# Optimization experiments

Hardware: AMD Instinct MI355X
Metric: run time of the kernel (lower is better)

Reference implementation:

```python
import jax, jax.numpy as jnp
import numpy as np

B, C, M, T = 2, 512, 16, 128
H = 8
D = C // H  # 64, divisible by 4 for 2D RoPE
G = C // 4  # GroupNorm groups = 128
S = M * T


def group_norm(x, scale, bias, groups=G, eps=1e-5):
    b, c, m, t = x.shape
    xg = x.reshape(b, groups, c // groups, m, t)
    mu = xg.mean(axis=(2, 3, 4), keepdims=True)
    var = xg.var(axis=(2, 3, 4), keepdims=True)
    xn = ((xg - mu) * jax.lax.rsqrt(var + eps)).reshape(b, c, m, t)
    return xn * scale[None, :, None, None] + bias[None, :, None, None]


def dwsep_conv(x, dw, pw):
    # depthwise 3x3 (groups=C) then pointwise 1x1
    y = jax.lax.conv_general_dilated(
        x, dw, window_strides=(1, 1), padding='SAME',
        dimension_numbers=('NCHW', 'HWIO', 'NCHW'), feature_group_count=x.shape[1])
    return jnp.einsum('bcmt,cd->bdmt', y, pw)


def rope2d(x):
    # x: [B,H,M,T,D]; first D/2 dims rotated by freq index m, last D/2 by time index t
    d = x.shape[-1]
    dh = d // 2
    q = dh // 2
    inv = 1.0 / (10000.0 ** (jnp.arange(q, dtype=jnp.float32) / q))

    def rot(v, ang):
        h = v.shape[-1] // 2
        v1, v2 = v[..., :h], v[..., h:]
        c, s = jnp.cos(ang), jnp.sin(ang)
        return jnp.concatenate([v1 * c - v2 * s, v1 * s + v2 * c], axis=-1)

    ang_f = jnp.arange(x.shape[2], dtype=jnp.float32)[:, None] * inv  # [M,q]
    ang_t = jnp.arange(x.shape[3], dtype=jnp.float32)[:, None] * inv  # [T,q]
    xf = rot(x[..., :dh], ang_f[:, None, :])  # broadcast over T
    xt = rot(x[..., dh:], ang_t)
    return jnp.concatenate([xf, xt], axis=-1)


def setup_inputs() -> dict:
    key = jax.random.key(0)
    ks = jax.random.split(key, 14)
    s = 0.02
    return {
        'x': jax.random.normal(ks[0], (B, C, M, T), jnp.float32),
        'lengths': jax.random.randint(ks[1], (B,), T // 2, T + 1),
        'gn_scale': jnp.ones((C,), jnp.float32),
        'gn_bias': jnp.zeros((C,), jnp.float32),
        'dw_q': jax.random.normal(ks[2], (3, 3, 1, C), jnp.float32) * s,
        'dw_k': jax.random.normal(ks[3], (3, 3, 1, C), jnp.float32) * s,
        'dw_v': jax.random.normal(ks[4], (3, 3, 1, C), jnp.float32) * s,
        'pw_q': jax.random.normal(ks[5], (C, C), jnp.float32) * s,
        'pw_k': jax.random.normal(ks[6], (C, C), jnp.float32) * s,
        'pw_v': jax.random.normal(ks[7], (C, C), jnp.float32) * s,
        'attn_w': jax.random.normal(ks[8], (C, C), jnp.float32) * s,
        'attn_b': jnp.zeros((C,), jnp.float32),
        'out_w': jax.random.normal(ks[9], (C, C), jnp.float32) * s,
        'out_b': jnp.zeros((C,), jnp.float32),
    }


def reference(x, lengths, gn_scale, gn_bias, dw_q, dw_k, dw_v, pw_q, pw_k, pw_v,
              attn_w, attn_b, out_w, out_b):
    residual = x
    xn = group_norm(x, gn_scale, gn_bias)

    def to_heads(y):  # [B,C,M,T] -> [B,H,M,T,D]
        return y.reshape(B, H, D, M, T).transpose(0, 1, 3, 4, 2)

    q = rope2d(to_heads(dwsep_conv(xn, dw_q, pw_q)))
    k = rope2d(to_heads(dwsep_conv(xn, dw_k, pw_k)))
    v = to_heads(dwsep_conv(xn, dw_v, pw_v))

    q = q.reshape(B, H, S, D)
    k = k.reshape(B, H, S, D)
    v = v.reshape(B, H, S, D)

    scores = jnp.einsum('bhsd,bhkd->bhsk', q, k) / np.sqrt(D).astype(np.float32)
    valid_t = jnp.arange(T)[None, :] < lengths[:, None]        # [B,T]
    valid = jnp.tile(valid_t, (1, M))                          # [B,S], token idx = m*T + t
    scores = jnp.where(valid[:, None, None, :], scores, jnp.float32(-1e9))
    attn = jax.nn.softmax(scores, axis=-1)
    o = jnp.einsum('bhsk,bhkd->bhsd', attn, v)                 # [B,H,S,D]

    o = o.transpose(0, 2, 1, 3).reshape(B, S, C)
    o = o @ attn_w + attn_b                                    # block output proj
    o = o.reshape(B, M, T, C).transpose(0, 3, 1, 2)            # [B,C,M,T]
    out = jnp.einsum('bcmt,cd->bdmt', o, out_w) + out_b[None, :, None, None]
    return residual + out
```

## Files before the change

kernel.cpp:

```cpp
#include <hip/hip_runtime.h>
#include <math.h>

#define CCH 512
#define SSQ 2048
#define MTOT 4096

typedef __bf16 bf16;
typedef __bf16 bf16x8 __attribute__((ext_vector_type(8)));
typedef __bf16 bf16x4 __attribute__((ext_vector_type(4)));
typedef float  f32x4  __attribute__((ext_vector_type(4)));

#define AS1 __attribute__((address_space(1)))
#define AS3 __attribute__((address_space(3)))
__device__ __forceinline__ void glds16(const void* g, void* l) {
    __builtin_amdgcn_global_load_lds((const AS1 void*)g, (AS3 void*)l, 16, 0, 0);
}

__global__ __launch_bounds__(256) void gnw_kernel(const float* __restrict__ x,
        float* __restrict__ mu, float* __restrict__ rstd,
        const float* __restrict__ w0, const float* __restrict__ w1,
        const float* __restrict__ w2, const float* __restrict__ w3,
        const float* __restrict__ w4, bf16* __restrict__ wT) {
    __shared__ float smem[64*65];
    int tid = threadIdx.x;
    if (blockIdx.x < 256) {
        float* s_sum = smem;
        float* s_sq  = smem + 256;
        int bg = blockIdx.x;
        long base = (long)bg * 8192;
        float sum = 0.f, sq = 0.f;
#pragma unroll
        for (int r = 0; r < 32; ++r) {
            float v = x[base + r*256 + tid];
            sum += v; sq += v*v;
        }
        s_sum[tid] = sum; s_sq[tid] = sq;
        __syncthreads();
        for (int off = 128; off > 0; off >>= 1) {
            if (tid < off) { s_sum[tid] += s_sum[tid+off]; s_sq[tid] += s_sq[tid+off]; }
            __syncthreads();
        }
        if (tid == 0) {
            float m = s_sum[0] * (1.f/8192.f);
            float v = s_sq[0]  * (1.f/8192.f) - m*m;
            mu[bg] = m;
            rstd[bg] = rsqrtf(v + 1e-5f);
        }
    } else {
        int bid = blockIdx.x - 256;
        int z = bid >> 6, r2 = bid & 63;
        int k0 = (r2 >> 3)*64, n0 = (r2 & 7)*64;
        const float* srcs[5] = {w0, w1, w2, w3, w4};
        const float* W = srcs[z];
        bf16* D = wT + (long)z * (CCH*CCH);
        float (*t)[65] = (float(*)[65])smem;
        int cI = tid & 63, r4 = tid >> 6;
#pragma unroll
        for (int p = 0; p < 16; ++p) {
            int kr = p*4 + r4;
            t[kr][cI] = W[(long)(k0+kr)*CCH + n0 + cI];
        }
        __syncthreads();
#pragma unroll
        for (int p = 0; p < 16; ++p) {
            int nr = p*4 + r4;
            D[(long)(n0+nr)*CCH + k0 + cI] = (bf16)t[cI][nr];
        }
    }
}

__global__ void tn_kernel(const float* __restrict__ x, const float* __restrict__ mu,
                          const float* __restrict__ rstd, const float* __restrict__ gsc,
                          const float* __restrict__ gbs, bf16* __restrict__ xnT) {
    __shared__ float t[64][65];
    int s0 = blockIdx.x*64, c0 = blockIdx.y*64, b = blockIdx.z;
    int tid = threadIdx.x;
    int cI = tid & 63, r4 = tid >> 6;
#pragma unroll
    for (int p = 0; p < 16; ++p) {
        int cr = p*4 + r4;
        t[cr][cI] = x[((long)(b*CCH + c0 + cr))*SSQ + s0 + cI];
    }
    __syncthreads();
#pragma unroll
    for (int p = 0; p < 16; ++p) {
        int sr = p*4 + r4;
        int c = c0 + cI;
        int g = b*128 + (c >> 2);
        float v = (t[cI][sr] - mu[g]) * rstd[g] * gsc[c] + gbs[c];
        xnT[((long)(b*SSQ + s0 + sr))*CCH + c] = (bf16)v;
    }
}

__global__ __launch_bounds__(256) void dw3_kernel(const bf16* __restrict__ xnT,
        const float* __restrict__ dwq, const float* __restrict__ dwk,
        const float* __restrict__ dwv,
        bf16* __restrict__ yq, bf16* __restrict__ yk, bf16* __restrict__ yv) {
    int tid = threadIdx.x;
    int cc = (tid & 63) * 8;
    int s  = blockIdx.x*4 + (tid >> 6);
    int sl = s & (SSQ-1);
    int b  = s >> 11;
    int m = sl >> 7, t = sl & 127;
    float aq[8] = {}, ak[8] = {}, av[8] = {};
#pragma unroll
    for (int di = 0; di < 3; ++di) {
        int m2 = m + di - 1;
        if ((unsigned)m2 >= 16u) continue;
#pragma unroll
        for (int dj = 0; dj < 3; ++dj) {
            int t2 = t + dj - 1;
            if ((unsigned)t2 >= 128u) continue;
            bf16x8 xv = *(const bf16x8*)(xnT + ((long)(b*SSQ + m2*128 + t2))*CCH + cc);
            int wi = (di*3 + dj)*CCH + cc;
#pragma unroll
            for (int i = 0; i < 8; ++i) {
                float xf = (float)xv[i];
                aq[i] += xf * dwq[wi+i];
                ak[i] += xf * dwk[wi+i];
                av[i] += xf * dwv[wi+i];
            }
        }
    }
    bf16x8 oq, ok, ov;
#pragma unroll
    for (int i = 0; i < 8; ++i) { oq[i] = (bf16)aq[i]; ok[i] = (bf16)ak[i]; ov[i] = (bf16)av[i]; }
    long o = (long)s*CCH + cc;
    *(bf16x8*)(yq + o) = oq;
    *(bf16x8*)(yk + o) = ok;
    *(bf16x8*)(yv + o) = ov;
}

template<int NFR>
__device__ __forceinline__ void gemm_core128(const bf16* __restrict__ A,
        const bf16* __restrict__ Wt, int m0, int n0,
        bf16* As, bf16* Bs, f32x4 (&acc)[4][NFR]) {
    int tid = threadIdx.x, lane = tid & 63, wid = tid >> 6;
    int sw = wid & 1, nw = wid >> 1;
    int col = lane & 15, quad = lane >> 4;
    const char* gA[4]; char* ldsA[4];
#pragma unroll
    for (int p = 0; p < 4; ++p) {
        int ci = tid + p*256;
        int row = ci >> 3;
        int c = (ci & 7) ^ (row & 7);
        gA[p] = (const char*)A + ((long)(m0+row)*CCH + c*8)*2;
        ldsA[p] = (char*)As + ci*16;
    }
    const char* gB[NFR]; char* ldsB[NFR];
#pragma unroll
    for (int p = 0; p < NFR; ++p) {
        int ci = tid + p*256;
        int row = ci >> 3;
        int c = (ci & 7) ^ (row & 7);
        gB[p] = (const char*)Wt + ((long)(n0+row)*CCH + c*8)*2;
        ldsB[p] = (char*)Bs + ci*16;
    }
    int rowA = sw*64 + col;
    int rowB = nw*(NFR*16) + col;
    for (int k0 = 0; k0 < CCH; k0 += 64) {
        __syncthreads();
#pragma unroll
        for (int p = 0; p < 4; ++p)   glds16(gA[p] + k0*2, ldsA[p]);
#pragma unroll
        for (int p = 0; p < NFR; ++p) glds16(gB[p] + k0*2, ldsB[p]);
        __syncthreads();
        bf16x8 af[4][2], bfr[NFR][2];
#pragma unroll
        for (int mt = 0; mt < 4; ++mt) {
            int r = rowA + mt*16;
#pragma unroll
            for (int ks = 0; ks < 2; ++ks) {
                int c = (ks*4 + quad) ^ (r & 7);
                af[mt][ks] = *(const bf16x8*)((char*)As + r*128 + c*16);
            }
        }
#pragma unroll
        for (int nt = 0; nt < NFR; ++nt) {
            int r = rowB + nt*16;
#pragma unroll
            for (int ks = 0; ks < 2; ++ks) {
                int c = (ks*4 + quad) ^ (r & 7);
                bfr[nt][ks] = *(const bf16x8*)((char*)Bs + r*128 + c*16);
            }
        }
#pragma unroll
        for (int ks = 0; ks < 2; ++ks)
#pragma unroll
            for (int mt = 0; mt < 4; ++mt)
#pragma unroll
                for (int nt = 0; nt < NFR; ++nt)
                    acc[mt][nt] = __builtin_amdgcn_mfma_f32_16x16x32_bf16(
                        af[mt][ks], bfr[nt][ks], acc[mt][nt], 0,0,0);
    }
}

__global__ __launch_bounds__(256) void gemm_qkv(const bf16* __restrict__ Abase,
        const bf16* __restrict__ wT, bf16* __restrict__ qout,
        bf16* __restrict__ kout, bf16* __restrict__ vout) {
    __shared__ bf16 As[128*64];
    __shared__ bf16 Bs[128*64];
    int m0 = blockIdx.x*128, n0 = blockIdx.y*128, z = blockIdx.z;
    f32x4 acc[4][4] = {};
    gemm_core128<4>(Abase + (long)z*MTOT*CCH, wT + (long)z*CCH*CCH, m0, n0, As, Bs, acc);
    int tid = threadIdx.x, lane = tid & 63, wid = tid >> 6;
    int sw = wid & 1, nw = wid >> 1;
    int col = lane & 15, quad = lane >> 4;
    int nbase = n0 + nw*64;
    int mb = m0 + sw*64;
    if (z < 2) {
        bf16* outp = z ? kout : qout;
        const float sc = z ? 1.0f : 0.125f;
        float invf = __expf(-(float)col * 0.5756462732485114f);
#pragma unroll
        for (int mt = 0; mt < 4; ++mt)
#pragma unroll
            for (int r = 0; r < 4; ++r) {
                int row = mb + mt*16 + quad*4 + r;
                int sl = row & (SSQ-1);
#pragma unroll
                for (int half = 0; half < 2; ++half) {
                    float pos = half ? (float)(sl & 127) : (float)(sl >> 7);
                    float ang = pos * invf;
                    float sn, cs;
                    __sincosf(ang, &sn, &cs);
                    float x1 = acc[mt][half*2+0][r], x2 = acc[mt][half*2+1][r];
                    outp[(long)row*CCH + nbase + half*32 + col]      = (bf16)((x1*cs - x2*sn)*sc);
                    outp[(long)row*CCH + nbase + half*32 + 16 + col] = (bf16)((x1*sn + x2*cs)*sc);
                }
            }
    } else {
#pragma unroll
        for (int mt = 0; mt < 4; ++mt)
#pragma unroll
            for (int nt = 0; nt < 4; ++nt) {
                int n = nbase + nt*16 + col;
                int row0 = mb + mt*16 + quad*4;
                int b = row0 >> 11, sl0 = row0 & (SSQ-1);
                bf16x4 pk;
#pragma unroll
                for (int r = 0; r < 4; ++r) pk[r] = (bf16)acc[mt][nt][r];
                *(bf16x4*)(vout + ((long)(b*CCH + n))*SSQ + sl0) = pk;
            }
    }
}

template<int MODE>
__global__ __launch_bounds__(256) void gemm_bf16(const bf16* __restrict__ A,
        const bf16* __restrict__ Wt, const float* __restrict__ bias,
        const float* __restrict__ resid, void* __restrict__ outv) {
    __shared__ bf16 As[128*64];
    __shared__ bf16 Bs[64*64];
    int m0 = blockIdx.x*128, n0 = blockIdx.y*64;
    f32x4 acc[4][2] = {};
    gemm_core128<2>(A, Wt, m0, n0, As, Bs, acc);
    int tid = threadIdx.x, lane = tid & 63, wid = tid >> 6;
    int sw = wid & 1, nw = wid >> 1;
    int col = lane & 15, quad = lane >> 4;
    int nb = n0 + nw*32, mb = m0 + sw*64;
    if (MODE == 3) {
        bf16* outp = (bf16*)outv;
#pragma unroll
        for (int nt = 0; nt < 2; ++nt) {
            int n = nb + nt*16 + col;
            float bv = bias[n];
#pragma unroll
            for (int mt = 0; mt < 4; ++mt)
#pragma unroll
                for (int r = 0; r < 4; ++r)
                    outp[(long)(mb + mt*16 + quad*4 + r)*CCH + n] = (bf16)(acc[mt][nt][r] + bv);
        }
    } else {
        float* outp = (float*)outv;
#pragma unroll
        for (int mt = 0; mt < 4; ++mt)
#pragma unroll
            for (int nt = 0; nt < 2; ++nt) {
                int n = nb + nt*16 + col;
                float bv = bias[n];
                int row0 = mb + mt*16 + quad*4;
                int b = row0 >> 11, sl0 = row0 & (SSQ-1);
                long off = ((long)(b*CCH + n))*SSQ + sl0;
                float4 rr = *(const float4*)(resid + off);
                float4 o4;
                o4.x = acc[mt][nt][0] + bv + rr.x;
                o4.y = acc[mt][nt][1] + bv + rr.y;
                o4.z = acc[mt][nt][2] + bv + rr.z;
                o4.w = acc[mt][nt][3] + bv + rr.w;
                *(float4*)(outp + off) = o4;
            }
    }
}

#define KIMG 8192
__global__ __launch_bounds__(256) void attn_kernel(
        const bf16* __restrict__ qb, const bf16* __restrict__ kb,
        const bf16* __restrict__ vb, const int* __restrict__ lengths,
        bf16* __restrict__ o) {
    __shared__ char KVs[2][2*KIMG];
    __shared__ bf16 Ps[4][16*72];
    int b = blockIdx.z, h = blockIdx.y;
    int tid = threadIdx.x, wid = tid >> 6, lane = tid & 63;
    int col = lane & 15, quad = lane >> 4;
    int q0 = blockIdx.x*64 + wid*16;
    int lenb = lengths[b];

    const char* gp[4]; long gstep[4]; int ldsoff[4];
#pragma unroll
    for (int p = 0; p < 4; ++p) {
        int idx = tid + p*256;
        int isV = idx >> 9;
        int rem = idx & 511;
        int r = rem >> 3;
        int csrc = (rem & 7) ^ (r & 7);
        if (!isV) { gp[p] = (const char*)kb + ((long)(b*SSQ + r))*1024 + h*128 + csrc*16; gstep[p] = 65536; }
        else      { gp[p] = (const char*)vb + ((long)(b*CCH + h*64 + r))*4096 + csrc*16;  gstep[p] = 128; }
        ldsoff[p] = idx*16;
    }

    f32x4 vm[2][4];
#pragma unroll
    for (int p2 = 0; p2 < 2; ++p2)
#pragma unroll
        for (int sub = 0; sub < 4; ++sub)
#pragma unroll
            for (int r = 0; r < 4; ++r)
                vm[p2][sub][r] = (p2*64 + sub*16 + quad*4 + r < lenb) ? 1.f : 0.f;

    const bf16* qp = qb + (long)(b*SSQ)*CCH + h*64;
    bf16x8 qf[2];
#pragma unroll
    for (int dc = 0; dc < 2; ++dc)
        qf[dc] = *(const bf16x8*)(qp + (long)(q0 + col)*CCH + dc*32 + quad*8);

    f32x4 of[4] = {};
    float lsum = 0.f;
    bf16* pw = Ps[wid];
    int cswz = col & 7;

    bf16x8 sreg[4];
#pragma unroll
    for (int p = 0; p < 4; ++p) sreg[p] = *(const bf16x8*)(gp[p]);
#pragma unroll
    for (int p = 0; p < 4; ++p) *(bf16x8*)(KVs[0] + ldsoff[p]) = sreg[p];
#pragma unroll
    for (int p = 0; p < 4; ++p) sreg[p] = *(const bf16x8*)(gp[p] + gstep[p]);
    __syncthreads();

    for (int t = 0; t < 32; ++t) {
        const bf16* K = (const bf16*)(KVs[t & 1]);
        const bf16* V = (const bf16*)(KVs[t & 1] + KIMG);
        int par = t & 1;
        f32x4 acc[4] = {};
#pragma unroll
        for (int sub = 0; sub < 4; ++sub)
#pragma unroll
            for (int dc = 0; dc < 2; ++dc) {
                bf16x8 kf = *(const bf16x8*)((const char*)K + (sub*16 + col)*128 + (((dc*4+quad) ^ cswz))*16);
                acc[sub] = __builtin_amdgcn_mfma_f32_16x16x32_bf16(kf, qf[dc], acc[sub], 0,0,0);
            }
#pragma unroll
        for (int sub = 0; sub < 4; ++sub) {
            bf16x4 pk;
#pragma unroll
            for (int r = 0; r < 4; ++r) {
                float p = __expf(acc[sub][r]) * vm[par][sub][r];
                lsum += p;
                pk[r] = (bf16)p;
            }
            *(bf16x4*)(pw + col*72 + sub*16 + quad*4) = pk;
        }
#pragma unroll
        for (int ks = 0; ks < 2; ++ks) {
            bf16x8 pf = *(const bf16x8*)(pw + col*72 + ks*32 + quad*8);
#pragma unroll
            for (int dt = 0; dt < 4; ++dt) {
                bf16x8 vf = *(const bf16x8*)((const char*)V + (dt*16 + col)*128 + (((ks*4+quad) ^ cswz))*16);
                of[dt] = __builtin_amdgcn_mfma_f32_16x16x32_bf16(pf, vf, of[dt], 0,0,0);
            }
        }
        if (t < 31) {
            char* nbuf = KVs[(t + 1) & 1];
#pragma unroll
            for (int p = 0; p < 4; ++p) *(bf16x8*)(nbuf + ldsoff[p]) = sreg[p];
            if (t < 30)
#pragma unroll
                for (int p = 0; p < 4; ++p)
                    sreg[p] = *(const bf16x8*)(gp[p] + (long)(t + 2) * gstep[p]);
        }
        __syncthreads();
    }
    lsum += __shfl_xor(lsum, 16);
    lsum += __shfl_xor(lsum, 32);
    float invl = 1.f / lsum;
    float ir[4];
#pragma unroll
    for (int r = 0; r < 4; ++r) ir[r] = __shfl(invl, quad*4 + r);
    bf16* ob = o + (long)(b*SSQ + q0)*CCH + h*64;
#pragma unroll
    for (int dt = 0; dt < 4; ++dt)
#pragma unroll
        for (int r = 0; r < 4; ++r)
            ob[(long)(quad*4 + r)*CCH + dt*16 + col] = (bf16)(of[dt][r] * ir[r]);
}

extern "C" void kernel_launch(void* const* d_in, const int* in_sizes, int n_in,
                              void* d_out, int out_size, void* d_ws, size_t ws_size,
                              hipStream_t stream) {
    const float* x        = (const float*)d_in[0];
    const int*   lengths  = (const int*)  d_in[1];
    const float* gn_scale = (const float*)d_in[2];
    const float* gn_bias  = (const float*)d_in[3];
    const float* dw_q     = (const float*)d_in[4];
    const float* dw_k     = (const float*)d_in[5];
    const float* dw_v     = (const float*)d_in[6];
    const float* pw_q     = (const float*)d_in[7];
    const float* pw_k     = (const float*)d_in[8];
    const float* pw_v     = (const float*)d_in[9];
    const float* attn_w   = (const float*)d_in[10];
    const float* attn_b   = (const float*)d_in[11];
    const float* out_w    = (const float*)d_in[12];
    const float* out_b    = (const float*)d_in[13];
    float* out = (float*)d_out;

    char* w = (char*)d_ws;
    float* mu   = (float*)w;
    float* rstd = (float*)(w + 1024);
    bf16* wT    = (bf16*)(w + 4096);
    bf16* wTa = wT + 3*CCH*CCH;
    bf16* wTo = wT + 4*CCH*CCH;
    bf16* xnT  = (bf16*)(w + 0x00300000);
    bf16* yT   = (bf16*)(w + 0x00700000);
    bf16* qbf  = (bf16*)(w + 0x01300000);
    bf16* kbf  = (bf16*)(w + 0x01700000);
    bf16* vbf  = (bf16*)(w + 0x01B00000);
    bf16* obf  = (bf16*)(w + 0x01F00000);
    bf16* tmpb = (bf16*)(w + 0x02300000);

    gnw_kernel<<<576, 256, 0, stream>>>(x, mu, rstd, pw_q, pw_k, pw_v, attn_w, out_w, wT);
    tn_kernel<<<dim3(32,8,2), 256, 0, stream>>>(x, mu, rstd, gn_scale, gn_bias, xnT);
    dw3_kernel<<<MTOT/4, 256, 0, stream>>>(xnT, dw_q, dw_k, dw_v,
                                           yT, yT + (long)MTOT*CCH, yT + (long)2*MTOT*CCH);

    gemm_qkv<<<dim3(MTOT/128, CCH/128, 3), 256, 0, stream>>>(yT, wT, qbf, kbf, vbf);

    attn_kernel<<<dim3(SSQ/64, 8, 2), 256, 0, stream>>>(qbf, kbf, vbf, lengths, obf);

    dim3 gg(MTOT/128, CCH/64);
    gemm_bf16<3><<<gg, 256, 0, stream>>>(obf, wTa, attn_b, nullptr, tmpb);
    gemm_bf16<4><<<gg, 256, 0, stream>>>(tmpb, wTo, out_b, x, out);
}
```

Baseline: 172.5 us.

## Split attention keys across warps with register-direct K/V loads; shrink QKV GEMM tile

The attention kernel now has each wave handle 32 queries against half of the 64 keys in each key tile. K and V fragments are loaded straight from global memory into registers with double buffering, so the LDS staging and per-tile block barriers are gone. The two key-halves are merged through shared memory at the end. Blocks are remapped so batch and head vary fastest, and the QKV GEMM uses 128x64 tiles, doubling its grid. The aim is fewer barriers, more parallelism and better L2 reuse, at the cost of duplicated global loads and more register pressure.

```diff
diff --git a/kernel.cpp b/kernel.cpp
--- a/kernel.cpp
+++ b/kernel.cpp
@@ -199,48 +199,45 @@
         const bf16* __restrict__ wT, bf16* __restrict__ qout,
         bf16* __restrict__ kout, bf16* __restrict__ vout) {
     __shared__ bf16 As[128*64];
-    __shared__ bf16 Bs[128*64];
-    int m0 = blockIdx.x*128, n0 = blockIdx.y*128, z = blockIdx.z;
-    f32x4 acc[4][4] = {};
-    gemm_core128<4>(Abase + (long)z*MTOT*CCH, wT + (long)z*CCH*CCH, m0, n0, As, Bs, acc);
+    __shared__ bf16 Bs[64*64];
+    int m0 = blockIdx.x*128, n0 = blockIdx.y*64, z = blockIdx.z;
+    f32x4 acc[4][2] = {};
+    gemm_core128<2>(Abase + (long)z*MTOT*CCH, wT + (long)z*CCH*CCH, m0, n0, As, Bs, acc);
     int tid = threadIdx.x, lane = tid & 63, wid = tid >> 6;
     int sw = wid & 1, nw = wid >> 1;
     int col = lane & 15, quad = lane >> 4;
-    int nbase = n0 + nw*64;
-    int mb = m0 + sw*64;
+    int nb = n0 + nw*32, mb = m0 + sw*64;
     if (z < 2) {
         bf16* outp = z ? kout : qout;
         const float sc = z ? 1.0f : 0.125f;
         float invf = __expf(-(float)col * 0.5756462732485114f);
+        bool tHalf = (nb & 32) != 0;
 #pragma unroll
         for (int mt = 0; mt < 4; ++mt)
 #pragma unroll
             for (int r = 0; r < 4; ++r) {
                 int row = mb + mt*16 + quad*4 + r;
                 int sl = row & (SSQ-1);
-#pragma unroll
-                for (int half = 0; half < 2; ++half) {
-                    float pos = half ? (float)(sl & 127) : (float)(sl >> 7);
-                    float ang = pos * invf;
-                    float sn, cs;
-                    __sincosf(ang, &sn, &cs);
-                    float x1 = acc[mt][half*2+0][r], x2 = acc[mt][half*2+1][r];
-                    outp[(long)row*CCH + nbase + half*32 + col]      = (bf16)((x1*cs - x2*sn)*sc);
-                    outp[(long)row*CCH + nbase + half*32 + 16 + col] = (bf16)((x1*sn + x2*cs)*sc);
-                }
+                float pos = tHalf ? (float)(sl & 127) : (float)(sl >> 7);
+                float ang = pos * invf;
+                float sn, cs;
+                __sincosf(ang, &sn, &cs);
+                float x1 = acc[mt][0][r], x2 = acc[mt][1][r];
+                outp[(long)row*CCH + nb + col]      = (bf16)((x1*cs - x2*sn)*sc);
+                outp[(long)row*CCH + nb + 16 + col] = (bf16)((x1*sn + x2*cs)*sc);
             }
     } else {
 #pragma unroll
         for (int mt = 0; mt < 4; ++mt)
 #pragma unroll
-            for (int nt = 0; nt < 4; ++nt) {
-                int n = nbase + nt*16 + col;
+            for (int nt = 0; nt < 2; ++nt) {
+                int n = nb + nt*16 + col;
                 int row0 = mb + mt*16 + quad*4;
-                int b = row0 >> 11, sl0 = row0 & (SSQ-1);
+                int bq = row0 >> 11, sl0 = row0 & (SSQ-1);
                 bf16x4 pk;
 #pragma unroll
                 for (int r = 0; r < 4; ++r) pk[r] = (bf16)acc[mt][nt][r];
-                *(bf16x4*)(vout + ((long)(b*CCH + n))*SSQ + sl0) = pk;
+                *(bf16x4*)(vout + ((long)(bq*CCH + n))*SSQ + sl0) = pk;
             }
     }
 }
@@ -292,116 +289,154 @@
     }
 }
 
-#define KIMG 8192
-__global__ __launch_bounds__(256) void attn_kernel(
+#define PSTR 40
+
+template<int MASKED>
+__device__ __forceinline__ void attn_tile(
+        const bf16x8 (&KC)[2][2], const bf16x8 (&VC)[4],
+        bf16x8 (&KN)[2][2], bf16x8 (&VN)[4], int tn,
+        const char* const (&kp)[2][2], const char* const (&vp)[4],
+        const bf16x8 (&qf)[2][2], const f32x4 (&vm)[2],
+        bf16* pw, int col, int quad,
+        f32x4 (&of)[2][4], float& ls0, float& ls1) {
+    if (tn < 32) {
+        long tko = (long)tn * 65536;
+#pragma unroll
+        for (int sub = 0; sub < 2; ++sub)
+#pragma unroll
+            for (int dc = 0; dc < 2; ++dc)
+                KN[sub][dc] = *(const bf16x8*)(kp[sub][dc] + tko);
+        long tvo = (long)tn * 128;
+#pragma unroll
+        for (int dt = 0; dt < 4; ++dt)
+            VN[dt] = *(const bf16x8*)(vp[dt] + tvo);
+    }
+    f32x4 sc[2][2] = {};
+#pragma unroll
+    for (int dc = 0; dc < 2; ++dc)
+#pragma unroll
+        for (int sub = 0; sub < 2; ++sub)
+#pragma unroll
+            for (int qt = 0; qt < 2; ++qt)
+                sc[sub][qt] = __builtin_amdgcn_mfma_f32_16x16x32_bf16(
+                    KC[sub][dc], qf[qt][dc], sc[sub][qt], 0,0,0);
+#pragma unroll
+    for (int sub = 0; sub < 2; ++sub)
+#pragma unroll
+        for (int qt = 0; qt < 2; ++qt) {
+            bf16x4 pk;
+#pragma unroll
+            for (int r = 0; r < 4; ++r) {
+                float p = __expf(sc[sub][qt][r]);
+                if (MASKED) p *= vm[sub][r];
+                if (qt) ls1 += p; else ls0 += p;
+                pk[r] = (bf16)p;
+            }
+            *(bf16x4*)(pw + (qt*16 + col)*PSTR + sub*16 + quad*4) = pk;
+        }
+    bf16x8 pf0 = *(const bf16x8*)(pw + col*PSTR + quad*8);
+    bf16x8 pf1 = *(const bf16x8*)(pw + (16 + col)*PSTR + quad*8);
+#pragma unroll
+    for (int dt = 0; dt < 4; ++dt) {
+        of[0][dt] = __builtin_amdgcn_mfma_f32_16x16x32_bf16(pf0, VC[dt], of[0][dt], 0,0,0);
+        of[1][dt] = __builtin_amdgcn_mfma_f32_16x16x32_bf16(pf1, VC[dt], of[1][dt], 0,0,0);
+    }
+}
+
+__global__ __launch_bounds__(256, 2) void attn_kernel(
         const bf16* __restrict__ qb, const bf16* __restrict__ kb,
         const bf16* __restrict__ vb, const int* __restrict__ lengths,
         bf16* __restrict__ o) {
-    __shared__ char KVs[2][2*KIMG];
-    __shared__ bf16 Ps[4][16*72];
-    int b = blockIdx.z, h = blockIdx.y;
+    __shared__ bf16 Ps[4][32*PSTR];
+    __shared__ float Om[2][2][4][16][17];
+    __shared__ float Lm[2][2][16];
+    int bid = blockIdx.x;
+    int bh = bid & 15, qtb = bid >> 4;
+    int h = bh >> 1, b = bh & 1;
     int tid = threadIdx.x, wid = tid >> 6, lane = tid & 63;
     int col = lane & 15, quad = lane >> 4;
-    int q0 = blockIdx.x*64 + wid*16;
+    int qh = wid & 1, kh = wid >> 1;
+    int q0 = qtb*64;
     int lenb = lengths[b];
 
-    const char* gp[4]; long gstep[4]; int ldsoff[4];
-#pragma unroll
-    for (int p = 0; p < 4; ++p) {
-        int idx = tid + p*256;
-        int isV = idx >> 9;
-        int rem = idx & 511;
-        int r = rem >> 3;
-        int csrc = (rem & 7) ^ (r & 7);
-        if (!isV) { gp[p] = (const char*)kb + ((long)(b*SSQ + r))*1024 + h*128 + csrc*16; gstep[p] = 65536; }
-        else      { gp[p] = (const char*)vb + ((long)(b*CCH + h*64 + r))*4096 + csrc*16;  gstep[p] = 128; }
-        ldsoff[p] = idx*16;
-    }
-
-    f32x4 vm[2][4];
-#pragma unroll
-    for (int p2 = 0; p2 < 2; ++p2)
-#pragma unroll
-        for (int sub = 0; sub < 4; ++sub)
-#pragma unroll
-            for (int r = 0; r < 4; ++r)
-                vm[p2][sub][r] = (p2*64 + sub*16 + quad*4 + r < lenb) ? 1.f : 0.f;
+    f32x4 vm[2];
+#pragma unroll
+    for (int sub = 0; sub < 2; ++sub)
+#pragma unroll
+        for (int r = 0; r < 4; ++r)
+            vm[sub][r] = (64 + kh*32 + sub*16 + quad*4 + r < lenb) ? 1.f : 0.f;
 
     const bf16* qp = qb + (long)(b*SSQ)*CCH + h*64;
-    bf16x8 qf[2];
-#pragma unroll
-    for (int dc = 0; dc < 2; ++dc)
-        qf[dc] = *(const bf16x8*)(qp + (long)(q0 + col)*CCH + dc*32 + quad*8);
-
-    f32x4 of[4] = {};
-    float lsum = 0.f;
+    bf16x8 qf[2][2];
+#pragma unroll
+    for (int qt = 0; qt < 2; ++qt)
+#pragma unroll
+        for (int dc = 0; dc < 2; ++dc)
+            qf[qt][dc] = *(const bf16x8*)(qp + (long)(q0 + qh*32 + qt*16 + col)*CCH + dc*32 + quad*8);
+
+    const char* kp[2][2];
+#pragma unroll
+    for (int sub = 0; sub < 2; ++sub)
+#pragma unroll
+        for (int dc = 0; dc < 2; ++dc)
+            kp[sub][dc] = (const char*)(kb + ((long)(b*SSQ + kh*32 + sub*16 + col))*CCH + h*64 + dc*32 + quad*8);
+    const char* vp[4];
+#pragma unroll
+    for (int dt = 0; dt < 4; ++dt)
+        vp[dt] = (const char*)(vb + ((long)(b*CCH + h*64 + dt*16 + col))*SSQ + kh*32 + quad*8);
+
+    f32x4 of[2][4] = {};
+    float ls0 = 0.f, ls1 = 0.f;
     bf16* pw = Ps[wid];
-    int cswz = col & 7;
-
-    bf16x8 sreg[4];
-#pragma unroll
-    for (int p = 0; p < 4; ++p) sreg[p] = *(const bf16x8*)(gp[p]);
-#pragma unroll
-    for (int p = 0; p < 4; ++p) *(bf16x8*)(KVs[0] + ldsoff[p]) = sreg[p];
-#pragma unroll
-    for (int p = 0; p < 4; ++p) sreg[p] = *(const bf16x8*)(gp[p] + gstep[p]);
+
+    bf16x8 kA[2][2], vA[4], kB[2][2], vB[4];
+#pragma unroll
+    for (int sub = 0; sub < 2; ++sub)
+#pragma unroll
+        for (int dc = 0; dc < 2; ++dc)
+            kA[sub][dc] = *(const bf16x8*)(kp[sub][dc]);
+#pragma unroll
+    for (int dt = 0; dt < 4; ++dt)
+        vA[dt] = *(const bf16x8*)(vp[dt]);
+
+    for (int t = 0; t < 32; t += 2) {
+        attn_tile<0>(kA, vA, kB, vB, t+1, kp, vp, qf, vm, pw, col, quad, of, ls0, ls1);
+        attn_tile<1>(kB, vB, kA, vA, t+2, kp, vp, qf, vm, pw, col, quad, of, ls0, ls1);
+    }
+
+    ls0 += __shfl_xor(ls0, 16); ls0 += __shfl_xor(ls0, 32);
+    ls1 += __shfl_xor(ls1, 16); ls1 += __shfl_xor(ls1, 32);
+
+    if (kh == 1) {
+#pragma unroll
+        for (int qt = 0; qt < 2; ++qt)
+#pragma unroll
+            for (int dt = 0; dt < 4; ++dt)
+#pragma unroll
+                for (int r = 0; r < 4; ++r)
+                    Om[qh][qt][dt][quad*4 + r][col] = of[qt][dt][r];
+        if (lane < 16) { Lm[qh][0][lane] = ls0; Lm[qh][1][lane] = ls1; }
+    }
     __syncthreads();
-
-    for (int t = 0; t < 32; ++t) {
-        const bf16* K = (const bf16*)(KVs[t & 1]);
-        const bf16* V = (const bf16*)(KVs[t & 1] + KIMG);
-        int par = t & 1;
-        f32x4 acc[4] = {};
-#pragma unroll
-        for (int sub = 0; sub < 4; ++sub)
-#pragma unroll
-            for (int dc = 0; dc < 2; ++dc) {
-                bf16x8 kf = *(const bf16x8*)((const char*)K + (sub*16 + col)*128 + (((dc*4+quad) ^ cswz))*16);
-                acc[sub] = __builtin_amdgcn_mfma_f32_16x16x32_bf16(kf, qf[dc], acc[sub], 0,0,0);
-            }
-#pragma unroll
-        for (int sub = 0; sub < 4; ++sub) {
-            bf16x4 pk;
-#pragma unroll
-            for (int r = 0; r < 4; ++r) {
-                float p = __expf(acc[sub][r]) * vm[par][sub][r];
-                lsum += p;
-                pk[r] = (bf16)p;
-            }
-            *(bf16x4*)(pw + col*72 + sub*16 + quad*4) = pk;
-        }
-#pragma unroll
-        for (int ks = 0; ks < 2; ++ks) {
-            bf16x8 pf = *(const bf16x8*)(pw + col*72 + ks*32 + quad*8);
-#pragma unroll
-            for (int dt = 0; dt < 4; ++dt) {
-                bf16x8 vf = *(const bf16x8*)((const char*)V + (dt*16 + col)*128 + (((ks*4+quad) ^ cswz))*16);
-                of[dt] = __builtin_amdgcn_mfma_f32_16x16x32_bf16(pf, vf, of[dt], 0,0,0);
-            }
-        }
-        if (t < 31) {
-            char* nbuf = KVs[(t + 1) & 1];
-#pragma unroll
-            for (int p = 0; p < 4; ++p) *(bf16x8*)(nbuf + ldsoff[p]) = sreg[p];
-            if (t < 30)
-#pragma unroll
-                for (int p = 0; p < 4; ++p)
-                    sreg[p] = *(const bf16x8*)(gp[p] + (long)(t + 2) * gstep[p]);
-        }
-        __syncthreads();
-    }
-    lsum += __shfl_xor(lsum, 16);
-    lsum += __shfl_xor(lsum, 32);
-    float invl = 1.f / lsum;
-    float ir[4];
-#pragma unroll
-    for (int r = 0; r < 4; ++r) ir[r] = __shfl(invl, quad*4 + r);
-    bf16* ob = o + (long)(b*SSQ + q0)*CCH + h*64;
-#pragma unroll
-    for (int dt = 0; dt < 4; ++dt)
-#pragma unroll
-        for (int r = 0; r < 4; ++r)
-            ob[(long)(quad*4 + r)*CCH + dt*16 + col] = (bf16)(of[dt][r] * ir[r]);
+    if (kh == 0) {
+        float i0 = 1.f / (ls0 + Lm[qh][0][col]);
+        float i1 = 1.f / (ls1 + Lm[qh][1][col]);
+        bf16* ob = o + (long)(b*SSQ + q0 + qh*32)*CCH + h*64;
+#pragma unroll
+        for (int qt = 0; qt < 2; ++qt) {
+            float inv = qt ? i1 : i0;
+            float ir[4];
+#pragma unroll
+            for (int r = 0; r < 4; ++r) ir[r] = __shfl(inv, quad*4 + r);
+#pragma unroll
+            for (int dt = 0; dt < 4; ++dt)
+#pragma unroll
+                for (int r = 0; r < 4; ++r) {
+                    float v = of[qt][dt][r] + Om[qh][qt][dt][quad*4 + r][col];
+                    ob[(long)(qt*16 + quad*4 + r)*CCH + dt*16 + col] = (bf16)(v * ir[r]);
+                }
+        }
+    }
 }
 
 extern "C" void kernel_launch(void* const* d_in, const int* in_sizes, int n_in,
@@ -442,9 +477,9 @@
     dw3_kernel<<<MTOT/4, 256, 0, stream>>>(xnT, dw_q, dw_k, dw_v,
                                            yT, yT + (long)MTOT*CCH, yT + (long)2*MTOT*CCH);
 
-    gemm_qkv<<<dim3(MTOT/128, CCH/128, 3), 256, 0, stream>>>(yT, wT, qbf, kbf, vbf);
-
-    attn_kernel<<<dim3(SSQ/64, 8, 2), 256, 0, stream>>>(qbf, kbf, vbf, lengths, obf);
+    gemm_qkv<<<dim3(MTOT/128, CCH/64, 3), 256, 0, stream>>>(yT, wT, qbf, kbf, vbf);
+
+    attn_kernel<<<512, 256, 0, stream>>>(qbf, kbf, vbf, lengths, obf);
 
     dim3 gg(MTOT/128, CCH/64);
     gemm_bf16<3><<<gg, 256, 0, stream>>>(obf, wTa, attn_b, nullptr, tmpb);
```

Measured after the change: 192.1 us. 11.3% more time.

## Split attention over KV halves, widen per-wave query tile, add merge kernel

Applied to the files above, without the earlier changes.

The attention kernel now splits the key range into two halves, giving 512 blocks over a flat grid. Each wave handles 32 queries, so every K/V fragment loaded from shared memory is reused twice. K/V tiles are loaded with asynchronous global-to-LDS loads, and the length mask becomes an additive bias applied only on masked tiles. A new merge kernel sums the fp32 partial outputs and row sums before normalising. The QKV GEMM is retiled to 128x64 for more blocks. The cost is extra fp32 partial traffic and one more launch.

```diff
diff --git a/kernel.cpp b/kernel.cpp
--- a/kernel.cpp
+++ b/kernel.cpp
@@ -199,48 +199,45 @@
         const bf16* __restrict__ wT, bf16* __restrict__ qout,
         bf16* __restrict__ kout, bf16* __restrict__ vout) {
     __shared__ bf16 As[128*64];
-    __shared__ bf16 Bs[128*64];
-    int m0 = blockIdx.x*128, n0 = blockIdx.y*128, z = blockIdx.z;
-    f32x4 acc[4][4] = {};
-    gemm_core128<4>(Abase + (long)z*MTOT*CCH, wT + (long)z*CCH*CCH, m0, n0, As, Bs, acc);
+    __shared__ bf16 Bs[64*64];
+    int m0 = blockIdx.x*128, n0 = blockIdx.y*64, z = blockIdx.z;
+    f32x4 acc[4][2] = {};
+    gemm_core128<2>(Abase + (long)z*MTOT*CCH, wT + (long)z*CCH*CCH, m0, n0, As, Bs, acc);
     int tid = threadIdx.x, lane = tid & 63, wid = tid >> 6;
     int sw = wid & 1, nw = wid >> 1;
     int col = lane & 15, quad = lane >> 4;
-    int nbase = n0 + nw*64;
-    int mb = m0 + sw*64;
+    int nb = n0 + nw*32, mb = m0 + sw*64;
     if (z < 2) {
         bf16* outp = z ? kout : qout;
         const float sc = z ? 1.0f : 0.125f;
         float invf = __expf(-(float)col * 0.5756462732485114f);
+        bool tHalf = (nb & 32) != 0;
 #pragma unroll
         for (int mt = 0; mt < 4; ++mt)
 #pragma unroll
             for (int r = 0; r < 4; ++r) {
                 int row = mb + mt*16 + quad*4 + r;
                 int sl = row & (SSQ-1);
-#pragma unroll
-                for (int half = 0; half < 2; ++half) {
-                    float pos = half ? (float)(sl & 127) : (float)(sl >> 7);
-                    float ang = pos * invf;
-                    float sn, cs;
-                    __sincosf(ang, &sn, &cs);
-                    float x1 = acc[mt][half*2+0][r], x2 = acc[mt][half*2+1][r];
-                    outp[(long)row*CCH + nbase + half*32 + col]      = (bf16)((x1*cs - x2*sn)*sc);
-                    outp[(long)row*CCH + nbase + half*32 + 16 + col] = (bf16)((x1*sn + x2*cs)*sc);
-                }
+                float pos = tHalf ? (float)(sl & 127) : (float)(sl >> 7);
+                float ang = pos * invf;
+                float sn, cs;
+                __sincosf(ang, &sn, &cs);
+                float x1 = acc[mt][0][r], x2 = acc[mt][1][r];
+                outp[(long)row*CCH + nb + col]      = (bf16)((x1*cs - x2*sn)*sc);
+                outp[(long)row*CCH + nb + 16 + col] = (bf16)((x1*sn + x2*cs)*sc);
             }
     } else {
 #pragma unroll
         for (int mt = 0; mt < 4; ++mt)
 #pragma unroll
-            for (int nt = 0; nt < 4; ++nt) {
-                int n = nbase + nt*16 + col;
+            for (int nt = 0; nt < 2; ++nt) {
+                int n = nb + nt*16 + col;
                 int row0 = mb + mt*16 + quad*4;
-                int b = row0 >> 11, sl0 = row0 & (SSQ-1);
+                int bq = row0 >> 11, sl0 = row0 & (SSQ-1);
                 bf16x4 pk;
 #pragma unroll
                 for (int r = 0; r < 4; ++r) pk[r] = (bf16)acc[mt][nt][r];
-                *(bf16x4*)(vout + ((long)(b*CCH + n))*SSQ + sl0) = pk;
+                *(bf16x4*)(vout + ((long)(bq*CCH + n))*SSQ + sl0) = pk;
             }
     }
 }
@@ -292,18 +289,22 @@
     }
 }
 
-#define KIMG 8192
 __global__ __launch_bounds__(256) void attn_kernel(
         const bf16* __restrict__ qb, const bf16* __restrict__ kb,
         const bf16* __restrict__ vb, const int* __restrict__ lengths,
-        bf16* __restrict__ o) {
-    __shared__ char KVs[2][2*KIMG];
-    __shared__ bf16 Ps[4][16*72];
-    int b = blockIdx.z, h = blockIdx.y;
+        float* __restrict__ opart, float* __restrict__ lpart) {
+    __shared__ char KV[2][16384];
+    __shared__ bf16 Ps[4][32*72];
+    int bid = blockIdx.x;
+    int bh = bid & 15;
+    int n  = bid >> 4;
+    int qt = n & 15, kvh = n >> 4;
+    int b = bh >> 3, h = bh & 7;
     int tid = threadIdx.x, wid = tid >> 6, lane = tid & 63;
     int col = lane & 15, quad = lane >> 4;
-    int q0 = blockIdx.x*64 + wid*16;
     int lenb = lengths[b];
+    int q0 = qt*128 + wid*32;
+    int k0 = kvh*1024;
 
     const char* gp[4]; long gstep[4]; int ldsoff[4];
 #pragma unroll
@@ -313,95 +314,122 @@
         int rem = idx & 511;
         int r = rem >> 3;
         int csrc = (rem & 7) ^ (r & 7);
-        if (!isV) { gp[p] = (const char*)kb + ((long)(b*SSQ + r))*1024 + h*128 + csrc*16; gstep[p] = 65536; }
-        else      { gp[p] = (const char*)vb + ((long)(b*CCH + h*64 + r))*4096 + csrc*16;  gstep[p] = 128; }
+        if (!isV) { gp[p] = (const char*)kb + ((long)(b*SSQ + k0 + r))*1024 + h*128 + csrc*16; gstep[p] = 65536; }
+        else      { gp[p] = (const char*)vb + ((long)(b*CCH + h*64 + r))*4096 + (long)k0*2 + csrc*16; gstep[p] = 128; }
         ldsoff[p] = idx*16;
     }
 
-    f32x4 vm[2][4];
-#pragma unroll
-    for (int p2 = 0; p2 < 2; ++p2)
-#pragma unroll
-        for (int sub = 0; sub < 4; ++sub)
-#pragma unroll
-            for (int r = 0; r < 4; ++r)
-                vm[p2][sub][r] = (p2*64 + sub*16 + quad*4 + r < lenb) ? 1.f : 0.f;
+    f32x4 mb[4];
+#pragma unroll
+    for (int sub = 0; sub < 4; ++sub)
+#pragma unroll
+        for (int r = 0; r < 4; ++r)
+            mb[sub][r] = (64 + sub*16 + quad*4 + r < lenb) ? 0.f : -10000.f;
 
     const bf16* qp = qb + (long)(b*SSQ)*CCH + h*64;
-    bf16x8 qf[2];
-#pragma unroll
-    for (int dc = 0; dc < 2; ++dc)
-        qf[dc] = *(const bf16x8*)(qp + (long)(q0 + col)*CCH + dc*32 + quad*8);
-
-    f32x4 of[4] = {};
-    float lsum = 0.f;
+    bf16x8 qf[2][2];
+#pragma unroll
+    for (int qt2 = 0; qt2 < 2; ++qt2)
+#pragma unroll
+        for (int dc = 0; dc < 2; ++dc)
+            qf[qt2][dc] = *(const bf16x8*)(qp + (long)(q0 + qt2*16 + col)*CCH + dc*32 + quad*8);
+
+    f32x4 of[2][4] = {};
+    float ls0 = 0.f, ls1 = 0.f;
     bf16* pw = Ps[wid];
     int cswz = col & 7;
 
-    bf16x8 sreg[4];
-#pragma unroll
-    for (int p = 0; p < 4; ++p) sreg[p] = *(const bf16x8*)(gp[p]);
-#pragma unroll
-    for (int p = 0; p < 4; ++p) *(bf16x8*)(KVs[0] + ldsoff[p]) = sreg[p];
-#pragma unroll
-    for (int p = 0; p < 4; ++p) sreg[p] = *(const bf16x8*)(gp[p] + gstep[p]);
+#pragma unroll
+    for (int p = 0; p < 4; ++p) glds16(gp[p], KV[0] + ldsoff[p]);
     __syncthreads();
 
-    for (int t = 0; t < 32; ++t) {
-        const bf16* K = (const bf16*)(KVs[t & 1]);
-        const bf16* V = (const bf16*)(KVs[t & 1] + KIMG);
-        int par = t & 1;
-        f32x4 acc[4] = {};
+    for (int t = 0; t < 16; ++t) {
+        if (t < 15) {
+#pragma unroll
+            for (int p = 0; p < 4; ++p)
+                glds16(gp[p] + (long)(t+1)*gstep[p], KV[(t+1) & 1] + ldsoff[p]);
+        }
+        const bf16* K = (const bf16*)(KV[t & 1]);
+        const bf16* V = (const bf16*)(KV[t & 1] + 8192);
+        bool masked = ((kvh*16 + t) & 1) != 0;
+        f32x4 sc[4][2];
+#pragma unroll
+        for (int sub = 0; sub < 4; ++sub)
+#pragma unroll
+            for (int qt2 = 0; qt2 < 2; ++qt2)
+                sc[sub][qt2] = masked ? mb[sub] : (f32x4){0.f,0.f,0.f,0.f};
 #pragma unroll
         for (int sub = 0; sub < 4; ++sub)
 #pragma unroll
             for (int dc = 0; dc < 2; ++dc) {
                 bf16x8 kf = *(const bf16x8*)((const char*)K + (sub*16 + col)*128 + (((dc*4+quad) ^ cswz))*16);
-                acc[sub] = __builtin_amdgcn_mfma_f32_16x16x32_bf16(kf, qf[dc], acc[sub], 0,0,0);
-            }
-#pragma unroll
-        for (int sub = 0; sub < 4; ++sub) {
-            bf16x4 pk;
-#pragma unroll
-            for (int r = 0; r < 4; ++r) {
-                float p = __expf(acc[sub][r]) * vm[par][sub][r];
-                lsum += p;
-                pk[r] = (bf16)p;
-            }
-            *(bf16x4*)(pw + col*72 + sub*16 + quad*4) = pk;
-        }
+#pragma unroll
+                for (int qt2 = 0; qt2 < 2; ++qt2)
+                    sc[sub][qt2] = __builtin_amdgcn_mfma_f32_16x16x32_bf16(
+                        kf, qf[qt2][dc], sc[sub][qt2], 0,0,0);
+            }
+#pragma unroll
+        for (int sub = 0; sub < 4; ++sub)
+#pragma unroll
+            for (int qt2 = 0; qt2 < 2; ++qt2) {
+                bf16x4 pk;
+#pragma unroll
+                for (int r = 0; r < 4; ++r) {
+                    float p = __expf(sc[sub][qt2][r]);
+                    if (qt2) ls1 += p; else ls0 += p;
+                    pk[r] = (bf16)p;
+                }
+                *(bf16x4*)(pw + (qt2*16 + col)*72 + sub*16 + quad*4) = pk;
+            }
 #pragma unroll
         for (int ks = 0; ks < 2; ++ks) {
-            bf16x8 pf = *(const bf16x8*)(pw + col*72 + ks*32 + quad*8);
+            bf16x8 pf0 = *(const bf16x8*)(pw + col*72 + ks*32 + quad*8);
+            bf16x8 pf1 = *(const bf16x8*)(pw + (16 + col)*72 + ks*32 + quad*8);
 #pragma unroll
             for (int dt = 0; dt < 4; ++dt) {
                 bf16x8 vf = *(const bf16x8*)((const char*)V + (dt*16 + col)*128 + (((ks*4+quad) ^ cswz))*16);
-                of[dt] = __builtin_amdgcn_mfma_f32_16x16x32_bf16(pf, vf, of[dt], 0,0,0);
-            }
-        }
-        if (t < 31) {
-            char* nbuf = KVs[(t + 1) & 1];
-#pragma unroll
-            for (int p = 0; p < 4; ++p) *(bf16x8*)(nbuf + ldsoff[p]) = sreg[p];
-            if (t < 30)
-#pragma unroll
-                for (int p = 0; p < 4; ++p)
-                    sreg[p] = *(const bf16x8*)(gp[p] + (long)(t + 2) * gstep[p]);
+                of[0][dt] = __builtin_amdgcn_mfma_f32_16x16x32_bf16(pf0, vf, of[0][dt], 0,0,0);
+                of[1][dt] = __builtin_amdgcn_mfma_f32_16x16x32_bf16(pf1, vf, of[1][dt], 0,0,0);
+            }
         }
         __syncthreads();
     }
-    lsum += __shfl_xor(lsum, 16);
-    lsum += __shfl_xor(lsum, 32);
-    float invl = 1.f / lsum;
-    float ir[4];
-#pragma unroll
-    for (int r = 0; r < 4; ++r) ir[r] = __shfl(invl, quad*4 + r);
-    bf16* ob = o + (long)(b*SSQ + q0)*CCH + h*64;
-#pragma unroll
-    for (int dt = 0; dt < 4; ++dt)
-#pragma unroll
-        for (int r = 0; r < 4; ++r)
-            ob[(long)(quad*4 + r)*CCH + dt*16 + col] = (bf16)(of[dt][r] * ir[r]);
+
+    ls0 += __shfl_xor(ls0, 16); ls0 += __shfl_xor(ls0, 32);
+    ls1 += __shfl_xor(ls1, 16); ls1 += __shfl_xor(ls1, 32);
+
+    float* op = opart + ((long)(kvh*16 + bh)*2048)*64;
+#pragma unroll
+    for (int qt2 = 0; qt2 < 2; ++qt2)
+#pragma unroll
+        for (int dt = 0; dt < 4; ++dt)
+#pragma unroll
+            for (int r = 0; r < 4; ++r)
+                op[(long)(q0 + qt2*16 + quad*4 + r)*64 + dt*16 + col] = of[qt2][dt][r];
+    if (quad == 0) {
+        float* lp = lpart + (long)(kvh*16 + bh)*2048;
+        lp[q0 + col]      = ls0;
+        lp[q0 + 16 + col] = ls1;
+    }
+}
+
+__global__ __launch_bounds__(256) void attn_merge(const float* __restrict__ opart,
+        const float* __restrict__ lpart, bf16* __restrict__ o) {
+    int idx = blockIdx.x*256 + threadIdx.x;
+    int dchunk = idx & 15;
+    int q = (idx >> 4) & 2047;
+    int bh = idx >> 15;
+    long o0 = ((long)bh*2048 + q)*64 + dchunk*4;
+    float4 a = *(const float4*)(opart + o0);
+    float4 c = *(const float4*)(opart + o0 + (long)16*2048*64);
+    float inv = 1.f / (lpart[bh*2048 + q] + lpart[(16 + bh)*2048 + q]);
+    bf16x4 pk;
+    pk[0] = (bf16)((a.x + c.x) * inv);
+    pk[1] = (bf16)((a.y + c.y) * inv);
+    pk[2] = (bf16)((a.z + c.z) * inv);
+    pk[3] = (bf16)((a.w + c.w) * inv);
+    int b = bh >> 3, h = bh & 7;
+    *(bf16x4*)(o + ((long)(b*SSQ + q))*CCH + h*64 + dchunk*4) = pk;
 }
 
 extern "C" void kernel_launch(void* const* d_in, const int* in_sizes, int n_in,
@@ -429,8 +457,10 @@
     bf16* wT    = (bf16*)(w + 4096);
     bf16* wTa = wT + 3*CCH*CCH;
     bf16* wTo = wT + 4*CCH*CCH;
+    float* lpart = (float*)(w + 0x00290000);
     bf16* xnT  = (bf16*)(w + 0x00300000);
     bf16* yT   = (bf16*)(w + 0x00700000);
+    float* opart = (float*)(w + 0x00300000);
     bf16* qbf  = (bf16*)(w + 0x01300000);
     bf16* kbf  = (bf16*)(w + 0x01700000);
     bf16* vbf  = (bf16*)(w + 0x01B00000);
@@ -442,9 +472,10 @@
     dw3_kernel<<<MTOT/4, 256, 0, stream>>>(xnT, dw_q, dw_k, dw_v,
                                            yT, yT + (long)MTOT*CCH, yT + (long)2*MTOT*CCH);
 
-    gemm_qkv<<<dim3(MTOT/128, CCH/128, 3), 256, 0, stream>>>(yT, wT, qbf, kbf, vbf);
-
-    attn_kernel<<<dim3(SSQ/64, 8, 2), 256, 0, stream>>>(qbf, kbf, vbf, lengths, obf);
+    gemm_qkv<<<dim3(MTOT/128, CCH/64, 3), 256, 0, stream>>>(yT, wT, qbf, kbf, vbf);
+
+    attn_kernel<<<512, 256, 0, stream>>>(qbf, kbf, vbf, lengths, opart, lpart);
+    attn_merge<<<2048, 256, 0, stream>>>(opart, lpart, obf);
 
     dim3 gg(MTOT/128, CCH/64);
     gemm_bf16<3><<<gg, 256, 0, stream>>>(obf, wTa, attn_b, nullptr, tmpb);
```

New measurement: 170.5 us. Within noise of the previous version (-1.2%).
